# Kernel optimization log

Hardware: AMD Instinct MI355X
Metric: run time of the kernel (lower is better)

The kernel has to match this reference:

```python
import jax, jax.numpy as jnp
import numpy as np

IN_CH = 64        # in_channels
MOD_H = 512       # modulation_hidden_dim
SIREN_H = 512     # siren_hidden_dim
NUM_PTS = 100
SCALE_INIT = 30.0  # SIREN first-layer frequency scale
N_STRANDS = 1024
NR_LAYERS = 3


def _wn_linear(x, v, g, b):
    # torch weight_norm(dim=0) on Linear: w = g * v / ||v||_row, row-wise over in-dim
    w = v * (g[:, None] / jnp.sqrt(jnp.sum(v * v, axis=1, keepdims=True)))
    return x @ w.T + b


def setup_inputs() -> dict:
    key = jax.random.key(0)
    ks = jax.random.split(key, 16)

    def p(k, shape, scale=0.05):
        return jax.random.normal(k, shape, dtype=jnp.float32) * scale

    inp = {"strand_features": p(ks[0], (N_STRANDS, IN_CH), 1.0)}
    mod_in = [IN_CH, MOD_H + IN_CH, MOD_H + IN_CH]
    for i in range(NR_LAYERS):
        inp[f"mod_v{i}"] = p(ks[1 + i], (MOD_H, mod_in[i]))
        inp[f"mod_g{i}"] = jnp.ones((MOD_H,), jnp.float32)
        inp[f"mod_b{i}"] = jnp.zeros((MOD_H,), jnp.float32)
    siren_in = [1, SIREN_H, SIREN_H]
    for i in range(NR_LAYERS):
        inp[f"siren_v{i}"] = p(ks[4 + i], (SIREN_H, siren_in[i]))
        inp[f"siren_g{i}"] = jnp.ones((SIREN_H,), jnp.float32)
        inp[f"siren_b{i}"] = jnp.zeros((SIREN_H,), jnp.float32)
    inp["dec_v"] = p(ks[7], (3, SIREN_H))
    inp["dec_g"] = jnp.ones((3,), jnp.float32)
    inp["dec_b"] = jnp.zeros((3,), jnp.float32)
    return inp


def reference(strand_features,
              mod_v0, mod_g0, mod_b0,
              mod_v1, mod_g1, mod_b1,
              mod_v2, mod_g2, mod_b2,
              siren_v0, siren_g0, siren_b0,
              siren_v1, siren_g1, siren_b1,
              siren_v2, siren_g2, siren_b2,
              dec_v, dec_g, dec_b):
    mods = [(mod_v0, mod_g0, mod_b0), (mod_v1, mod_g1, mod_b1), (mod_v2, mod_g2, mod_b2)]
    sirens = [(siren_v0, siren_g0, siren_b0), (siren_v1, siren_g1, siren_b1), (siren_v2, siren_g2, siren_b2)]

    n = strand_features.shape[0]
    nv = NUM_PTS - 1  # decode_random_verts=False, decode_direct_xyz=False
    # t = linspace(0,1,num_pts)[0:num_pts-1], shape (N, nv, 1)
    t = jnp.linspace(0.0, 1.0, NUM_PTS, dtype=jnp.float32)[:nv].reshape(1, nv, 1)
    h_siren = jnp.broadcast_to(t, (n, nv, 1))
    z_initial = jnp.broadcast_to(strand_features[:, None, :], (n, nv, IN_CH))  # z_scaling = 1.0
    z = z_initial
    for i in range(NR_LAYERS):
        h_mod = jax.nn.silu(_wn_linear(z, *mods[i]))       # (n, nv, MOD_H)
        s = _wn_linear(h_siren, *sirens[i])                # (n, nv, SIREN_H)
        s = jnp.sin(SCALE_INIT * s) if i == 0 else jnp.sin(s)
        h_siren = (1.0 - h_mod) * s                        # FiLM-style gating
        z = jnp.concatenate([z_initial, h_mod], axis=2)    # (n, nv, IN_CH+MOD_H)
    hair_dir = _wn_linear(h_siren, dec_v, dec_g, dec_b) * 0.01  # (n, nv, 3)
    pred = jnp.cumsum(hair_dir, axis=1)
    start = jnp.zeros((n, 1, 3), jnp.float32)
    return jnp.concatenate([start, pred], axis=1)  # (n, NUM_PTS, 3)
```

## Files before the change

kernel.cpp:

```cpp
#include <hip/hip_runtime.h>
#include <math.h>

#define NS 1024
#define NV 99
#define NPTS 100
#define H 512

typedef __bf16 bf16x8 __attribute__((ext_vector_type(8)));
typedef __bf16 bf16x4 __attribute__((ext_vector_type(4)));
typedef float f32x4 __attribute__((ext_vector_type(4)));

#define GLD_LDS16(gp, lp) __builtin_amdgcn_global_load_lds(                 \
    (const __attribute__((address_space(1))) void*)(gp),                    \
    (__attribute__((address_space(3))) void*)(lp), 16, 0, 0)
#define WAIT_VM0()   __builtin_amdgcn_s_waitcnt(0x0f70)
#define WAIT_LGKM0() __builtin_amdgcn_s_waitcnt(0xc07f)

__global__ __launch_bounds__(256) void k_wnorm(
    const float* __restrict__ mv0, const float* __restrict__ mg0,
    const float* __restrict__ mv1, const float* __restrict__ mg1,
    const float* __restrict__ mv2, const float* __restrict__ mg2,
    const float* __restrict__ sv1, const float* __restrict__ sg1,
    const float* __restrict__ sv2, const float* __restrict__ sg2,
    const float* __restrict__ dv,  const float* __restrict__ dg,
    float* __restrict__ wnM0, float* __restrict__ wnM1, float* __restrict__ wnM2,
    __bf16* __restrict__ W1s, __bf16* __restrict__ W2s, float* __restrict__ wnD)
{
    int rid = blockIdx.x, tid = threadIdx.x;
    const float* src; const float* g; int len, j;
    float* dstf = nullptr; __bf16* dstb = nullptr;
    if (rid < 512)       { j = rid;        src = mv0 + j*64;  g = mg0; dstf = wnM0 + j*64;  len = 64;  }
    else if (rid < 1024) { j = rid - 512;  src = mv1 + j*576; g = mg1; dstf = wnM1 + j*576; len = 576; }
    else if (rid < 1536) { j = rid - 1024; src = mv2 + j*576; g = mg2; dstf = wnM2 + j*576; len = 576; }
    else if (rid < 2048) { j = rid - 1536; src = sv1 + j*512; g = sg1; dstb = W1s;          len = 512; }
    else if (rid < 2560) { j = rid - 2048; src = sv2 + j*512; g = sg2; dstb = W2s;          len = 512; }
    else                 { j = rid - 2560; src = dv  + j*512; g = dg;  dstf = wnD + j*512;  len = 512; }

    float ss = 0.f;
    for (int k = tid; k < len; k += 256) { float v = src[k]; ss += v * v; }
    __shared__ float red[4];
    __shared__ float s_scale;
    for (int o = 32; o > 0; o >>= 1) ss += __shfl_down(ss, o);
    if ((tid & 63) == 0) red[tid >> 6] = ss;
    __syncthreads();
    if (tid == 0) s_scale = g[j] * rsqrtf(red[0] + red[1] + red[2] + red[3]);
    __syncthreads();
    float sc = s_scale;
    if (dstb) {
        for (int k = tid; k < len; k += 256) {
            int f  = (j >> 4) * 16 + (k >> 5);
            int el = ((f * 64) + ((k >> 3) & 3) * 16 + (j & 15)) * 8 + (k & 7);
            dstb[el] = (__bf16)(src[k] * sc);
        }
    } else {
        for (int k = tid; k < len; k += 256) dstf[k] = src[k] * sc;
    }
}

__global__ __launch_bounds__(256) void k_s0(
    const float* __restrict__ sv0, const float* __restrict__ sg0,
    const float* __restrict__ sb0, float* __restrict__ s0sin)
{
    int idx = blockIdx.x * 256 + threadIdx.x;
    if (idx >= NV * H) return;
    int p = idx >> 9, j = idx & 511;
    float v = sv0[j];
    float w = sg0[j] * v * rsqrtf(v * v);
    float t = (float)p / 99.0f;
    s0sin[idx] = __sinf(30.0f * (t * w + sb0[j]));
}

__global__ __launch_bounds__(256) void k_mod(
    const float* __restrict__ sf,
    const float* __restrict__ wnM0, const float* __restrict__ mb0,
    const float* __restrict__ wnM1, const float* __restrict__ mb1,
    const float* __restrict__ wnM2, const float* __restrict__ mb2,
    float* __restrict__ onem)
{
    const int g0 = blockIdx.x * 4, tid = threadIdx.x;
    __shared__ float z[4][576];

    for (int idx = tid; idx < 4 * 64; idx += 256)
        z[idx >> 6][idx & 63] = sf[(g0 + (idx >> 6)) * 64 + (idx & 63)];
    __syncthreads();

    float mreg[2][4];
#pragma unroll
    for (int r = 0; r < 2; ++r) {
        const int j = tid + 256 * r;
        const float* wr = wnM0 + j * 64;
        float acc[4] = {0.f, 0.f, 0.f, 0.f};
#pragma unroll
        for (int k = 0; k < 64; k += 4) {
            float4 w = *(const float4*)(wr + k);
#pragma unroll
            for (int g = 0; g < 4; ++g) {
                float4 zv = *(const float4*)&z[g][k];
                acc[g] += zv.x * w.x + zv.y * w.y + zv.z * w.z + zv.w * w.w;
            }
        }
        const float b = mb0[j];
#pragma unroll
        for (int g = 0; g < 4; ++g) {
            float a = acc[g] + b;
            float m = a / (1.f + __expf(-a));
            onem[(g0 + g) * H + j] = 1.f - m;
            mreg[r][g] = m;
        }
    }
    __syncthreads();
#pragma unroll
    for (int r = 0; r < 2; ++r)
#pragma unroll
        for (int g = 0; g < 4; ++g) z[g][64 + tid + 256 * r] = mreg[r][g];
    __syncthreads();

#pragma unroll
    for (int r = 0; r < 2; ++r) {
        const int j = tid + 256 * r;
        const float* wr = wnM1 + j * 576;
        float acc[4] = {0.f, 0.f, 0.f, 0.f};
        for (int k = 0; k < 576; k += 4) {
            float4 w = *(const float4*)(wr + k);
#pragma unroll
            for (int g = 0; g < 4; ++g) {
                float4 zv = *(const float4*)&z[g][k];
                acc[g] += zv.x * w.x + zv.y * w.y + zv.z * w.z + zv.w * w.w;
            }
        }
        const float b = mb1[j];
#pragma unroll
        for (int g = 0; g < 4; ++g) {
            float a = acc[g] + b;
            float m = a / (1.f + __expf(-a));
            onem[NS * H + (g0 + g) * H + j] = 1.f - m;
            mreg[r][g] = m;
        }
    }
    __syncthreads();
#pragma unroll
    for (int r = 0; r < 2; ++r)
#pragma unroll
        for (int g = 0; g < 4; ++g) z[g][64 + tid + 256 * r] = mreg[r][g];
    __syncthreads();

#pragma unroll
    for (int r = 0; r < 2; ++r) {
        const int j = tid + 256 * r;
        const float* wr = wnM2 + j * 576;
        float acc[4] = {0.f, 0.f, 0.f, 0.f};
        for (int k = 0; k < 576; k += 4) {
            float4 w = *(const float4*)(wr + k);
#pragma unroll
            for (int g = 0; g < 4; ++g) {
                float4 zv = *(const float4*)&z[g][k];
                acc[g] += zv.x * w.x + zv.y * w.y + zv.z * w.z + zv.w * w.w;
            }
        }
        const float b = mb2[j];
#pragma unroll
        for (int g = 0; g < 4; ++g) {
            float a = acc[g] + b;
            float m = a / (1.f + __expf(-a));
            onem[2 * NS * H + (g0 + g) * H + j] = 1.f - m;
        }
    }
}

__global__ __launch_bounds__(64, 1) void k_main(
    const __bf16* __restrict__ W1s, const __bf16* __restrict__ W2s,
    const float* __restrict__ wnD, const float* __restrict__ sb1,
    const float* __restrict__ sb2, const float* __restrict__ db,
    const float* __restrict__ s0sin, const float* __restrict__ onem,
    float* __restrict__ dirs)
{
    __shared__ __attribute__((aligned(16))) __bf16 h2p[32][520];
    __shared__ __attribute__((aligned(16))) __bf16 wst[8192];
    const int lane = threadIdx.x;
    const int L = lane & 15, Q = lane >> 4;
    const int base = blockIdx.x * 32;
    const int r0 = base + L, r1 = r0 + 16;
    const int s0 = r0 / 99, p0 = r0 - s0 * 99;
    const int s1 = r1 / 99, p1 = r1 - s1 * 99;

    bf16x8 Bh0[16], Bh1[16];
    {
        const float* omA = onem + s0 * H;
        const float* tsA = s0sin + p0 * H;
        const float* omB = onem + s1 * H;
        const float* tsB = s0sin + p1 * H;
#pragma unroll
        for (int t = 0; t < 16; ++t) {
            const int k0 = t * 32 + Q * 8;
            f32x4 oa = *(const f32x4*)(omA + k0);
            f32x4 ob = *(const f32x4*)(omA + k0 + 4);
            f32x4 ta = *(const f32x4*)(tsA + k0);
            f32x4 tb = *(const f32x4*)(tsA + k0 + 4);
            bf16x8 v;
            v[0] = (__bf16)(oa[0] * ta[0]); v[1] = (__bf16)(oa[1] * ta[1]);
            v[2] = (__bf16)(oa[2] * ta[2]); v[3] = (__bf16)(oa[3] * ta[3]);
            v[4] = (__bf16)(ob[0] * tb[0]); v[5] = (__bf16)(ob[1] * tb[1]);
            v[6] = (__bf16)(ob[2] * tb[2]); v[7] = (__bf16)(ob[3] * tb[3]);
            Bh0[t] = v;
            oa = *(const f32x4*)(omB + k0);
            ob = *(const f32x4*)(omB + k0 + 4);
            ta = *(const f32x4*)(tsB + k0);
            tb = *(const f32x4*)(tsB + k0 + 4);
            v[0] = (__bf16)(oa[0] * ta[0]); v[1] = (__bf16)(oa[1] * ta[1]);
            v[2] = (__bf16)(oa[2] * ta[2]); v[3] = (__bf16)(oa[3] * ta[3]);
            v[4] = (__bf16)(ob[0] * tb[0]); v[5] = (__bf16)(ob[1] * tb[1]);
            v[6] = (__bf16)(ob[2] * tb[2]); v[7] = (__bf16)(ob[3] * tb[3]);
            Bh1[t] = v;
        }
    }

    {
        const float* om1a = onem + NS * H + s0 * H;
        const float* om1b = onem + NS * H + s1 * H;
#pragma unroll 1
        for (int kb = 0; kb < 16; ++kb) {
            const __bf16* gpA = W1s + (size_t)kb * 16384 + (size_t)lane * 8;
            WAIT_LGKM0();
#pragma unroll
            for (int t = 0; t < 16; ++t)
                GLD_LDS16(gpA + t * 512, &wst[t * 512]);
            WAIT_VM0();
            f32x4 a00 = {0.f,0.f,0.f,0.f}, a01 = {0.f,0.f,0.f,0.f};
#pragma unroll
            for (int t = 0; t < 16; ++t) {
                bf16x8 w = *(const bf16x8*)&wst[t * 512 + lane * 8];
                a00 = __builtin_amdgcn_mfma_f32_16x16x32_bf16(w, Bh0[t], a00, 0, 0, 0);
                a01 = __builtin_amdgcn_mfma_f32_16x16x32_bf16(w, Bh1[t], a01, 0, 0, 0);
            }
            const __bf16* gpB = gpA + 16 * 512;
            WAIT_LGKM0();
#pragma unroll
            for (int t = 0; t < 16; ++t)
                GLD_LDS16(gpB + t * 512, &wst[t * 512]);
            WAIT_VM0();
            f32x4 a10 = {0.f,0.f,0.f,0.f}, a11 = {0.f,0.f,0.f,0.f};
#pragma unroll
            for (int t = 0; t < 16; ++t) {
                bf16x8 w = *(const bf16x8*)&wst[t * 512 + lane * 8];
                a10 = __builtin_amdgcn_mfma_f32_16x16x32_bf16(w, Bh0[t], a10, 0, 0, 0);
                a11 = __builtin_amdgcn_mfma_f32_16x16x32_bf16(w, Bh1[t], a11, 0, 0, 0);
            }
            const int c0 = kb * 32 + Q * 4, c1 = c0 + 16;
            float4 bi0 = *(const float4*)(sb1 + c0);
            float4 bi1 = *(const float4*)(sb1 + c1);
            float4 ga0 = *(const float4*)(om1a + c0);
            float4 ga1 = *(const float4*)(om1a + c1);
            float4 gb0 = *(const float4*)(om1b + c0);
            float4 gb1 = *(const float4*)(om1b + c1);
            bf16x4 v;
            v[0] = (__bf16)(ga0.x * __sinf(a00[0] + bi0.x));
            v[1] = (__bf16)(ga0.y * __sinf(a00[1] + bi0.y));
            v[2] = (__bf16)(ga0.z * __sinf(a00[2] + bi0.z));
            v[3] = (__bf16)(ga0.w * __sinf(a00[3] + bi0.w));
            *(bf16x4*)&h2p[L][c0] = v;
            v[0] = (__bf16)(ga1.x * __sinf(a10[0] + bi1.x));
            v[1] = (__bf16)(ga1.y * __sinf(a10[1] + bi1.y));
            v[2] = (__bf16)(ga1.z * __sinf(a10[2] + bi1.z));
            v[3] = (__bf16)(ga1.w * __sinf(a10[3] + bi1.w));
            *(bf16x4*)&h2p[L][c1] = v;
            v[0] = (__bf16)(gb0.x * __sinf(a01[0] + bi0.x));
            v[1] = (__bf16)(gb0.y * __sinf(a01[1] + bi0.y));
            v[2] = (__bf16)(gb0.z * __sinf(a01[2] + bi0.z));
            v[3] = (__bf16)(gb0.w * __sinf(a01[3] + bi0.w));
            *(bf16x4*)&h2p[16 + L][c0] = v;
            v[0] = (__bf16)(gb1.x * __sinf(a11[0] + bi1.x));
            v[1] = (__bf16)(gb1.y * __sinf(a11[1] + bi1.y));
            v[2] = (__bf16)(gb1.z * __sinf(a11[2] + bi1.z));
            v[3] = (__bf16)(gb1.w * __sinf(a11[3] + bi1.w));
            *(bf16x4*)&h2p[16 + L][c1] = v;
        }
    }
    __syncthreads();

#pragma unroll
    for (int t = 0; t < 16; ++t) {
        Bh0[t] = *(const bf16x8*)&h2p[L][t * 32 + Q * 8];
        Bh1[t] = *(const bf16x8*)&h2p[16 + L][t * 32 + Q * 8];
    }

    float pA0 = 0.f, pA1 = 0.f, pA2 = 0.f;
    float pB0 = 0.f, pB1 = 0.f, pB2 = 0.f;
    {
        const float* om2a = onem + 2 * NS * H + s0 * H;
        const float* om2b = onem + 2 * NS * H + s1 * H;
#pragma unroll 1
        for (int kb = 0; kb < 16; ++kb) {
            const __bf16* gpA = W2s + (size_t)kb * 16384 + (size_t)lane * 8;
            WAIT_LGKM0();
#pragma unroll
            for (int t = 0; t < 16; ++t)
                GLD_LDS16(gpA + t * 512, &wst[t * 512]);
            WAIT_VM0();
            f32x4 a00 = {0.f,0.f,0.f,0.f}, a01 = {0.f,0.f,0.f,0.f};
#pragma unroll
            for (int t = 0; t < 16; ++t) {
                bf16x8 w = *(const bf16x8*)&wst[t * 512 + lane * 8];
                a00 = __builtin_amdgcn_mfma_f32_16x16x32_bf16(w, Bh0[t], a00, 0, 0, 0);
                a01 = __builtin_amdgcn_mfma_f32_16x16x32_bf16(w, Bh1[t], a01, 0, 0, 0);
            }
            const __bf16* gpB = gpA + 16 * 512;
            WAIT_LGKM0();
#pragma unroll
            for (int t = 0; t < 16; ++t)
                GLD_LDS16(gpB + t * 512, &wst[t * 512]);
            WAIT_VM0();
            f32x4 a10 = {0.f,0.f,0.f,0.f}, a11 = {0.f,0.f,0.f,0.f};
#pragma unroll
            for (int t = 0; t < 16; ++t) {
                bf16x8 w = *(const bf16x8*)&wst[t * 512 + lane * 8];
                a10 = __builtin_amdgcn_mfma_f32_16x16x32_bf16(w, Bh0[t], a10, 0, 0, 0);
                a11 = __builtin_amdgcn_mfma_f32_16x16x32_bf16(w, Bh1[t], a11, 0, 0, 0);
            }
            const int c0 = kb * 32 + Q * 4, c1 = c0 + 16;
            float4 bi0 = *(const float4*)(sb2 + c0);
            float4 bi1 = *(const float4*)(sb2 + c1);
            float4 d00 = *(const float4*)(wnD + c0);
            float4 d10 = *(const float4*)(wnD + H + c0);
            float4 d20 = *(const float4*)(wnD + 2 * H + c0);
            float4 d01 = *(const float4*)(wnD + c1);
            float4 d11 = *(const float4*)(wnD + H + c1);
            float4 d21 = *(const float4*)(wnD + 2 * H + c1);
            float h;
            {
                float4 ga = *(const float4*)(om2a + c0);
                float4 gb = *(const float4*)(om2a + c1);
                h = ga.x * __sinf(a00[0] + bi0.x); pA0 += h * d00.x; pA1 += h * d10.x; pA2 += h * d20.x;
                h = ga.y * __sinf(a00[1] + bi0.y); pA0 += h * d00.y; pA1 += h * d10.y; pA2 += h * d20.y;
                h = ga.z * __sinf(a00[2] + bi0.z); pA0 += h * d00.z; pA1 += h * d10.z; pA2 += h * d20.z;
                h = ga.w * __sinf(a00[3] + bi0.w); pA0 += h * d00.w; pA1 += h * d10.w; pA2 += h * d20.w;
                h = gb.x * __sinf(a10[0] + bi1.x); pA0 += h * d01.x; pA1 += h * d11.x; pA2 += h * d21.x;
                h = gb.y * __sinf(a10[1] + bi1.y); pA0 += h * d01.y; pA1 += h * d11.y; pA2 += h * d21.y;
                h = gb.z * __sinf(a10[2] + bi1.z); pA0 += h * d01.z; pA1 += h * d11.z; pA2 += h * d21.z;
                h = gb.w * __sinf(a10[3] + bi1.w); pA0 += h * d01.w; pA1 += h * d11.w; pA2 += h * d21.w;
            }
            {
                float4 ga = *(const float4*)(om2b + c0);
                float4 gb = *(const float4*)(om2b + c1);
                h = ga.x * __sinf(a01[0] + bi0.x); pB0 += h * d00.x; pB1 += h * d10.x; pB2 += h * d20.x;
                h = ga.y * __sinf(a01[1] + bi0.y); pB0 += h * d00.y; pB1 += h * d10.y; pB2 += h * d20.y;
                h = ga.z * __sinf(a01[2] + bi0.z); pB0 += h * d00.z; pB1 += h * d10.z; pB2 += h * d20.z;
                h = ga.w * __sinf(a01[3] + bi0.w); pB0 += h * d00.w; pB1 += h * d10.w; pB2 += h * d20.w;
                h = gb.x * __sinf(a11[0] + bi1.x); pB0 += h * d01.x; pB1 += h * d11.x; pB2 += h * d21.x;
                h = gb.y * __sinf(a11[1] + bi1.y); pB0 += h * d01.y; pB1 += h * d11.y; pB2 += h * d21.y;
                h = gb.z * __sinf(a11[2] + bi1.z); pB0 += h * d01.z; pB1 += h * d11.z; pB2 += h * d21.z;
                h = gb.w * __sinf(a11[3] + bi1.w); pB0 += h * d01.w; pB1 += h * d11.w; pB2 += h * d21.w;
            }
        }
    }

    pA0 += __shfl_xor(pA0, 16, 64); pA0 += __shfl_xor(pA0, 32, 64);
    pA1 += __shfl_xor(pA1, 16, 64); pA1 += __shfl_xor(pA1, 32, 64);
    pA2 += __shfl_xor(pA2, 16, 64); pA2 += __shfl_xor(pA2, 32, 64);
    pB0 += __shfl_xor(pB0, 16, 64); pB0 += __shfl_xor(pB0, 32, 64);
    pB1 += __shfl_xor(pB1, 16, 64); pB1 += __shfl_xor(pB1, 32, 64);
    pB2 += __shfl_xor(pB2, 16, 64); pB2 += __shfl_xor(pB2, 32, 64);
    if (Q == 0) {
        const float d0 = db[0], d1 = db[1], d2 = db[2];
        dirs[r0 * 3 + 0] = 0.01f * (pA0 + d0);
        dirs[r0 * 3 + 1] = 0.01f * (pA1 + d1);
        dirs[r0 * 3 + 2] = 0.01f * (pA2 + d2);
        dirs[r1 * 3 + 0] = 0.01f * (pB0 + d0);
        dirs[r1 * 3 + 1] = 0.01f * (pB1 + d1);
        dirs[r1 * 3 + 2] = 0.01f * (pB2 + d2);
    }
}

__global__ __launch_bounds__(256) void k_cumsum(const float* __restrict__ dirs,
                                                float* __restrict__ out)
{
    const int wid = blockIdx.x * 4 + (threadIdx.x >> 6);
    const int lane = threadIdx.x & 63;
    const int s = wid / 3, c = wid - 3 * s;
    const float* dp = dirs + (size_t)s * NV * 3 + c;
    float v0 = dp[lane * 3];
    float v1 = (lane < NV - 64) ? dp[(64 + lane) * 3] : 0.f;
#pragma unroll
    for (int off = 1; off < 64; off <<= 1) {
        float t = __shfl_up(v0, off, 64);
        if (lane >= off) v0 += t;
        t = __shfl_up(v1, off, 64);
        if (lane >= off) v1 += t;
    }
    float tot0 = __shfl(v0, 63, 64);
    v1 += tot0;
    float* op = out + (size_t)s * NPTS * 3 + c;
    if (lane == 0) op[0] = 0.f;
    op[(lane + 1) * 3] = v0;
    if (lane < NV - 64) op[(64 + lane + 1) * 3] = v1;
}

extern "C" void kernel_launch(void* const* d_in, const int* in_sizes, int n_in,
                              void* d_out, int out_size, void* d_ws, size_t ws_size,
                              hipStream_t stream)
{
    const float* sf  = (const float*)d_in[0];
    const float* mv0 = (const float*)d_in[1];  const float* mg0 = (const float*)d_in[2];  const float* mb0 = (const float*)d_in[3];
    const float* mv1 = (const float*)d_in[4];  const float* mg1 = (const float*)d_in[5];  const float* mb1 = (const float*)d_in[6];
    const float* mv2 = (const float*)d_in[7];  const float* mg2 = (const float*)d_in[8];  const float* mb2 = (const float*)d_in[9];
    const float* sv0 = (const float*)d_in[10]; const float* sg0 = (const float*)d_in[11]; const float* sb0 = (const float*)d_in[12];
    const float* sv1 = (const float*)d_in[13]; const float* sg1 = (const float*)d_in[14]; const float* sb1 = (const float*)d_in[15];
    const float* sv2 = (const float*)d_in[16]; const float* sg2 = (const float*)d_in[17]; const float* sb2 = (const float*)d_in[18];
    const float* dv  = (const float*)d_in[19]; const float* dg  = (const float*)d_in[20]; const float* dbv = (const float*)d_in[21];

    float* ws = (float*)d_ws;
    float* wnM0  = ws;
    float* wnM1  = ws + 32768;
    float* wnM2  = ws + 327680;
    float* wnD   = ws + 622592;
    float* s0sin = ws + 624128;
    float* onem  = ws + 674816;
    float* dirs  = ws + 2247680;
    __bf16* W1s  = (__bf16*)(ws + 2551808);
    __bf16* W2s  = W1s + 262144;

    hipLaunchKernelGGL(k_wnorm, dim3(2563), dim3(256), 0, stream,
                       mv0, mg0, mv1, mg1, mv2, mg2, sv1, sg1, sv2, sg2, dv, dg,
                       wnM0, wnM1, wnM2, W1s, W2s, wnD);
    hipLaunchKernelGGL(k_s0, dim3(198), dim3(256), 0, stream, sv0, sg0, sb0, s0sin);
    hipLaunchKernelGGL(k_mod, dim3(256), dim3(256), 0, stream,
                       sf, wnM0, mb0, wnM1, mb1, wnM2, mb2, onem);
    hipLaunchKernelGGL(k_main, dim3((NS * NV) / 32), dim3(64), 0, stream,
                       W1s, W2s, wnD, sb1, sb2, dbv, s0sin, onem, dirs);
    hipLaunchKernelGGL(k_cumsum, dim3(768), dim3(256), 0, stream, dirs, (float*)d_out);
}
```

Before: 473.3 us.

## Double-buffer weight staging in LDS to prefetch next chunk during MFMA

Splits the single 16 KB LDS weight staging buffer into two 8 KB halves and streams each layer's weights in 4096-element chunks. The next chunk is issued with global_load_lds before computing on the current one, and a partial vmcnt wait lets the previous chunk finish while the new loads stay in flight. The first chunk of the layer-2 weights is also prefetched before the h2p reload, and the block-wide barrier becomes an LDS-count wait, which is enough since the block is a single wave. The goal is to hide global load latency behind the MFMA work. In exchange it relies on exact waitcnt accounting, and it overwrites a buffer that the previous iteration's LDS reads may still be using.

```diff
diff --git a/kernel.cpp b/kernel.cpp
--- a/kernel.cpp
+++ b/kernel.cpp
@@ -14,6 +14,7 @@
     (const __attribute__((address_space(1))) void*)(gp),                    \
     (__attribute__((address_space(3))) void*)(lp), 16, 0, 0)
 #define WAIT_VM0()   __builtin_amdgcn_s_waitcnt(0x0f70)
+#define WAIT_VM8()   __builtin_amdgcn_s_waitcnt(0x0f78)
 #define WAIT_LGKM0() __builtin_amdgcn_s_waitcnt(0xc07f)
 
 __global__ __launch_bounds__(256) void k_wnorm(
@@ -175,7 +176,8 @@
     float* __restrict__ dirs)
 {
     __shared__ __attribute__((aligned(16))) __bf16 h2p[32][520];
-    __shared__ __attribute__((aligned(16))) __bf16 wst[8192];
+    __shared__ __attribute__((aligned(16))) __bf16 wstA[4096];
+    __shared__ __attribute__((aligned(16))) __bf16 wstB[4096];
     const int lane = threadIdx.x;
     const int L = lane & 15, Q = lane >> 4;
     const int base = blockIdx.x * 32;
@@ -217,33 +219,43 @@
     {
         const float* om1a = onem + NS * H + s0 * H;
         const float* om1b = onem + NS * H + s1 * H;
+        {
+            const __bf16* gp = W1s + (size_t)lane * 8;
+#pragma unroll
+            for (int i = 0; i < 8; ++i) GLD_LDS16(gp + i * 512, &wstA[i * 512]);
+        }
 #pragma unroll 1
         for (int kb = 0; kb < 16; ++kb) {
-            const __bf16* gpA = W1s + (size_t)kb * 16384 + (size_t)lane * 8;
-            WAIT_LGKM0();
-#pragma unroll
-            for (int t = 0; t < 16; ++t)
-                GLD_LDS16(gpA + t * 512, &wst[t * 512]);
-            WAIT_VM0();
             f32x4 a00 = {0.f,0.f,0.f,0.f}, a01 = {0.f,0.f,0.f,0.f};
-#pragma unroll
-            for (int t = 0; t < 16; ++t) {
-                bf16x8 w = *(const bf16x8*)&wst[t * 512 + lane * 8];
-                a00 = __builtin_amdgcn_mfma_f32_16x16x32_bf16(w, Bh0[t], a00, 0, 0, 0);
-                a01 = __builtin_amdgcn_mfma_f32_16x16x32_bf16(w, Bh1[t], a01, 0, 0, 0);
-            }
-            const __bf16* gpB = gpA + 16 * 512;
-            WAIT_LGKM0();
-#pragma unroll
-            for (int t = 0; t < 16; ++t)
-                GLD_LDS16(gpB + t * 512, &wst[t * 512]);
-            WAIT_VM0();
             f32x4 a10 = {0.f,0.f,0.f,0.f}, a11 = {0.f,0.f,0.f,0.f};
 #pragma unroll
-            for (int t = 0; t < 16; ++t) {
-                bf16x8 w = *(const bf16x8*)&wst[t * 512 + lane * 8];
-                a10 = __builtin_amdgcn_mfma_f32_16x16x32_bf16(w, Bh0[t], a10, 0, 0, 0);
-                a11 = __builtin_amdgcn_mfma_f32_16x16x32_bf16(w, Bh1[t], a11, 0, 0, 0);
+            for (int q = 0; q < 4; ++q) {
+                const int f = kb * 4 + q;
+                const __bf16* cur = (f & 1) ? wstB : wstA;
+                if (f < 63) {
+                    __bf16* nxt = (f & 1) ? wstA : wstB;
+                    const __bf16* gp = W1s + (size_t)(f + 1) * 4096 + (size_t)lane * 8;
+#pragma unroll
+                    for (int i = 0; i < 8; ++i) GLD_LDS16(gp + i * 512, &nxt[i * 512]);
+                    WAIT_VM8();
+                } else {
+                    WAIT_VM0();
+                }
+                if (q < 2) {
+#pragma unroll
+                    for (int i = 0; i < 8; ++i) {
+                        bf16x8 w = *(const bf16x8*)&cur[i * 512 + lane * 8];
+                        a00 = __builtin_amdgcn_mfma_f32_16x16x32_bf16(w, Bh0[q * 8 + i], a00, 0, 0, 0);
+                        a01 = __builtin_amdgcn_mfma_f32_16x16x32_bf16(w, Bh1[q * 8 + i], a01, 0, 0, 0);
+                    }
+                } else {
+#pragma unroll
+                    for (int i = 0; i < 8; ++i) {
+                        bf16x8 w = *(const bf16x8*)&cur[i * 512 + lane * 8];
+                        a10 = __builtin_amdgcn_mfma_f32_16x16x32_bf16(w, Bh0[(q - 2) * 8 + i], a10, 0, 0, 0);
+                        a11 = __builtin_amdgcn_mfma_f32_16x16x32_bf16(w, Bh1[(q - 2) * 8 + i], a11, 0, 0, 0);
+                    }
+                }
             }
             const int c0 = kb * 32 + Q * 4, c1 = c0 + 16;
             float4 bi0 = *(const float4*)(sb1 + c0);
@@ -275,7 +287,13 @@
             *(bf16x4*)&h2p[16 + L][c1] = v;
         }
     }
-    __syncthreads();
+    WAIT_LGKM0();
+
+    {
+        const __bf16* gp = W2s + (size_t)lane * 8;
+#pragma unroll
+        for (int i = 0; i < 8; ++i) GLD_LDS16(gp + i * 512, &wstA[i * 512]);
+    }
 
 #pragma unroll
     for (int t = 0; t < 16; ++t) {
@@ -290,31 +308,36 @@
         const float* om2b = onem + 2 * NS * H + s1 * H;
 #pragma unroll 1
         for (int kb = 0; kb < 16; ++kb) {
-            const __bf16* gpA = W2s + (size_t)kb * 16384 + (size_t)lane * 8;
-            WAIT_LGKM0();
-#pragma unroll
-            for (int t = 0; t < 16; ++t)
-                GLD_LDS16(gpA + t * 512, &wst[t * 512]);
-            WAIT_VM0();
             f32x4 a00 = {0.f,0.f,0.f,0.f}, a01 = {0.f,0.f,0.f,0.f};
-#pragma unroll
-            for (int t = 0; t < 16; ++t) {
-                bf16x8 w = *(const bf16x8*)&wst[t * 512 + lane * 8];
-                a00 = __builtin_amdgcn_mfma_f32_16x16x32_bf16(w, Bh0[t], a00, 0, 0, 0);
-                a01 = __builtin_amdgcn_mfma_f32_16x16x32_bf16(w, Bh1[t], a01, 0, 0, 0);
-            }
-            const __bf16* gpB = gpA + 16 * 512;
-            WAIT_LGKM0();
-#pragma unroll
-            for (int t = 0; t < 16; ++t)
-                GLD_LDS16(gpB + t * 512, &wst[t * 512]);
-            WAIT_VM0();
             f32x4 a10 = {0.f,0.f,0.f,0.f}, a11 = {0.f,0.f,0.f,0.f};
 #pragma unroll
-            for (int t = 0; t < 16; ++t) {
-                bf16x8 w = *(const bf16x8*)&wst[t * 512 + lane * 8];
-                a10 = __builtin_amdgcn_mfma_f32_16x16x32_bf16(w, Bh0[t], a10, 0, 0, 0);
-                a11 = __builtin_amdgcn_mfma_f32_16x16x32_bf16(w, Bh1[t], a11, 0, 0, 0);
+            for (int q = 0; q < 4; ++q) {
+                const int f = kb * 4 + q;
+                const __bf16* cur = (f & 1) ? wstB : wstA;
+                if (f < 63) {
+                    __bf16* nxt = (f & 1) ? wstA : wstB;
+                    const __bf16* gp = W2s + (size_t)(f + 1) * 4096 + (size_t)lane * 8;
+#pragma unroll
+                    for (int i = 0; i < 8; ++i) GLD_LDS16(gp + i * 512, &nxt[i * 512]);
+                    WAIT_VM8();
+                } else {
+                    WAIT_VM0();
+                }
+                if (q < 2) {
+#pragma unroll
+                    for (int i = 0; i < 8; ++i) {
+                        bf16x8 w = *(const bf16x8*)&cur[i * 512 + lane * 8];
+                        a00 = __builtin_amdgcn_mfma_f32_16x16x32_bf16(w, Bh0[q * 8 + i], a00, 0, 0, 0);
+                        a01 = __builtin_amdgcn_mfma_f32_16x16x32_bf16(w, Bh1[q * 8 + i], a01, 0, 0, 0);
+                    }
+                } else {
+#pragma unroll
+                    for (int i = 0; i < 8; ++i) {
+                        bf16x8 w = *(const bf16x8*)&cur[i * 512 + lane * 8];
+                        a10 = __builtin_amdgcn_mfma_f32_16x16x32_bf16(w, Bh0[(q - 2) * 8 + i], a10, 0, 0, 0);
+                        a11 = __builtin_amdgcn_mfma_f32_16x16x32_bf16(w, Bh1[(q - 2) * 8 + i], a11, 0, 0, 0);
+                    }
+                }
             }
             const int c0 = kb * 32 + Q * 4, c1 = c0 + 16;
             float4 bi0 = *(const float4*)(sb2 + c0);
```

After: 501.2 us. 1.06x slower.
